# Performance work log

Measured on AMD Instinct MI355X. Metric: run time of the kernel, lower is better.

Reference implementation:

```python
import jax, jax.numpy as jnp
import numpy as np

N_NODES = 100000
N_EDGES = 1600000
IN_FEATS = 64
HIDDEN = 32
OUT_FEATS = 40


def _linear_init(key, fan_in, fan_out):
    kw, kb = jax.random.split(key)
    bound = 1.0 / np.sqrt(fan_in)
    W = jax.random.uniform(kw, (fan_in, fan_out), jnp.float32, -bound, bound)
    b = jax.random.uniform(kb, (fan_out,), jnp.float32, -bound, bound)
    return W, b


def setup_inputs() -> dict:
    key = jax.random.key(0)
    ks = jax.random.split(key, 8)
    x = jax.random.normal(ks[0], (N_NODES, IN_FEATS), jnp.float32)
    edge_index = jax.random.randint(ks[1], (2, N_EDGES), 0, N_NODES, jnp.int64)
    W_self1, b_self1 = _linear_init(ks[2], IN_FEATS, HIDDEN)
    W_neigh1, b_neigh1 = _linear_init(ks[3], IN_FEATS, HIDDEN)
    W_self2, b_self2 = _linear_init(ks[4], HIDDEN, HIDDEN)
    W_neigh2, b_neigh2 = _linear_init(ks[5], HIDDEN, HIDDEN)
    W_out, b_out = _linear_init(ks[6], HIDDEN, OUT_FEATS)
    W_lin1, b_lin1 = _linear_init(ks[7], IN_FEATS, OUT_FEATS)
    return {"x": x, "edge_index": edge_index,
            "W_self1": W_self1, "b_self1": b_self1,
            "W_neigh1": W_neigh1, "b_neigh1": b_neigh1,
            "W_self2": W_self2, "b_self2": b_self2,
            "W_neigh2": W_neigh2, "b_neigh2": b_neigh2,
            "W_out": W_out, "b_out": b_out,
            "W_lin1": W_lin1, "b_lin1": b_lin1}


def _scatter_mean(feats, src, dst, num_nodes):
    # gather neighbor features [E, F], sum into destinations, divide by degree
    msgs = feats[src]
    agg = jax.ops.segment_sum(msgs, dst, num_segments=num_nodes)
    cnt = jax.ops.segment_sum(jnp.ones((src.shape[0],), feats.dtype), dst,
                              num_segments=num_nodes)
    return agg / jnp.maximum(cnt, 1.0)[:, None]


def _intra_conv(h, src, dst, W_self, b_self, W_neigh, b_neigh, num_nodes):
    # scatter-mean aggregation + fused linear/residual(self)/relu
    x_self = h @ W_self + b_self
    neigh = _scatter_mean(h, src, dst, num_nodes)
    out = neigh @ W_neigh + b_neigh + x_self
    return jax.nn.relu(out)


def reference(x, edge_index, W_self1, b_self1, W_neigh1, b_neigh1,
              W_self2, b_self2, W_neigh2, b_neigh2, W_out, b_out,
              W_lin1, b_lin1):
    num_nodes = x.shape[0]
    src, dst = edge_index[0], edge_index[1]  # PyG source_to_target flow
    initial_x = x @ W_lin1 + b_lin1  # computed in original forward (unused in output)
    h = _intra_conv(x, src, dst, W_self1, b_self1, W_neigh1, b_neigh1, num_nodes)
    h = _intra_conv(h, src, dst, W_self2, b_self2, W_neigh2, b_neigh2, num_nodes)
    # hidden dim == 32 so x32 is the last layer's output (== h); dropout is eval no-op
    x32 = h
    logits = h @ W_out + b_out
    return (x32, logits)
```

## Files before the change

### kernel.cpp

```cpp
#include <hip/hip_runtime.h>

#define NN 100000
#define NE 1600000
#define RB 256
#define NPB 391
#define CAP 8192

typedef unsigned int uint;
typedef unsigned short ushort;
typedef __fp16 fp16x2 __attribute__((ext_vector_type(2)));

__device__ __forceinline__ float blo(uint u){ return __uint_as_float(u << 16); }
__device__ __forceinline__ float bhi(uint u){ return __uint_as_float(u & 0xffff0000u); }
__device__ __forceinline__ float b2f(ushort u){ return __uint_as_float(((uint)u) << 16); }
__device__ __forceinline__ ushort f2b(float f){
  uint u = __float_as_uint(f);
  uint r = (u + 0x7fffu + ((u >> 16) & 1u)) >> 16;
  return (ushort)r;
}
__device__ __forceinline__ uint packh2(float a, float b){
  union { fp16x2 h; uint u; } c; c.h = __builtin_amdgcn_cvt_pkrtz(a, b); return c.u;
}
__device__ __forceinline__ float h2lo(uint u){
  union { uint u; fp16x2 h; } c; c.u = u; return (float)c.h.x;
}
__device__ __forceinline__ float h2hi(uint u){
  union { uint u; fp16x2 h; } c; c.u = u; return (float)c.h.y;
}
__device__ __forceinline__ float ldf(const void* p, int i, bool isb){
  return isb ? b2f(((const ushort*)p)[i]) : ((const float*)p)[i];
}

__global__ void prep_k(const uint* __restrict__ xw,  const int* __restrict__ ei,
                       const void* __restrict__ Ws1, const void* __restrict__ bs1,
                       const void* __restrict__ Wn1, const void* __restrict__ bn1,
                       const void* __restrict__ Ws2, const void* __restrict__ bs2,
                       const void* __restrict__ Wn2, const void* __restrict__ bn2,
                       const void* __restrict__ Wo,  const void* __restrict__ bo,
                       float* __restrict__ wc1, float* __restrict__ bc1,
                       float* __restrict__ wc2, float* __restrict__ bc2,
                       float* __restrict__ wof, float* __restrict__ bof,
                       float* __restrict__ bn1f, float* __restrict__ bn2f,
                       int* __restrict__ flags, int* __restrict__ gcur)
{
  int t = threadIdx.x;
  __shared__ int nz, bcnt;
  __shared__ int s_isb, s_ei64;
  if (t == 0) { nz = 0; bcnt = 0; }
  __syncthreads();

  int hiw = ei[2 * t + 1];
  if (hiw != 0) atomicOr(&nz, 1);

  uint u = xw[t];
  uint le = (u >> 7) & 0xFFu;
  if (le == 0u || (le >= 96u && le <= 144u)) atomicAdd(&bcnt, 1);
  __syncthreads();
  if (t == 0) {
    s_ei64 = (nz == 0) ? 1 : 0;
    s_isb  = (bcnt >= 240) ? 1 : 0;
    flags[0] = s_isb;
    flags[1] = s_ei64;
  }
  __syncthreads();
  bool isb = (s_isb != 0);

  gcur[t] = t * CAP;

  for (int i = t; i < 64 * 64; i += 256) {
    int f = i >> 6, j = i & 63;
    wc1[i] = (j < 32) ? ldf(Ws1, f * 32 + j, isb) : ldf(Wn1, f * 32 + (j - 32), isb);
  }
  for (int i = t; i < 64; i += 256) bc1[i] = (i < 32) ? ldf(bs1, i, isb) : 0.f;
  for (int i = t; i < 32 * 64; i += 256) {
    int f = i >> 6, j = i & 63;
    wc2[i] = (j < 32) ? ldf(Ws2, f * 32 + j, isb) : ldf(Wn2, f * 32 + (j - 32), isb);
  }
  for (int i = t; i < 64; i += 256) bc2[i] = (i < 32) ? ldf(bs2, i, isb) : 0.f;
  for (int i = t; i < 32 * 40; i += 256) wof[i] = ldf(Wo, i, isb);
  for (int i = t; i < 40; i += 256) bof[i] = ldf(bo, i, isb);
  for (int i = t; i < 32; i += 256) bn1f[i] = ldf(bn1, i, isb);
  for (int i = t; i < 32; i += 256) bn2f[i] = ldf(bn2, i, isb);
}

__global__ __launch_bounds__(256) void part_k(const int* __restrict__ ei,
                                              const int* __restrict__ flags,
                                              int2* __restrict__ pairs,
                                              int* __restrict__ gcur, int E)
{
  __shared__ int hist[RB];
  __shared__ int gbase[RB];
  int m = flags[1];
  int base = blockIdx.x * 2048;
  hist[threadIdx.x] = 0;
  __syncthreads();
  int bk[8], rk[8]; int2 prs[8];
#pragma unroll
  for (int k = 0; k < 8; k++) {
    int e = base + threadIdx.x + k * 256;
    bk[k] = -1;
    if (e < E) {
      int d = m ? ei[2 * (E + e)] : ei[E + e];
      int s = m ? ei[2 * e] : ei[e];
      bk[k] = d / NPB;
      rk[k] = atomicAdd(&hist[bk[k]], 1);
      prs[k] = make_int2(d, s);
    }
  }
  __syncthreads();
  if (hist[threadIdx.x] > 0)
    gbase[threadIdx.x] = atomicAdd(&gcur[threadIdx.x], hist[threadIdx.x]);
  __syncthreads();
#pragma unroll
  for (int k = 0; k < 8; k++) {
    if (bk[k] >= 0) {
      int pos = gbase[bk[k]] + rk[k];
      if (pos < (bk[k] + 1) * CAP) pairs[pos] = prs[k];
    }
  }
}

__global__ void boffscan_k(const int* __restrict__ gcur, int* __restrict__ cnt,
                           int* __restrict__ boff, int* __restrict__ rowptr, int E)
{
  __shared__ int ps[RB];
  int t = threadIdx.x;
  int c = min(gcur[t] - t * CAP, CAP);
  cnt[t] = c;
  ps[t] = c;
  __syncthreads();
  for (int off = 1; off < RB; off <<= 1) {
    int v = (t >= off) ? ps[t - off] : 0;
    __syncthreads();
    ps[t] += v;
    __syncthreads();
  }
  boff[t] = ps[t] - c;
  if (t == RB - 1) rowptr[NN] = E;
}

__global__ __launch_bounds__(512) void csr_bucket_k(const int2* __restrict__ pairs,
                                                    const int* __restrict__ cnt,
                                                    const int* __restrict__ boff,
                                                    int* __restrict__ rowptr,
                                                    int* __restrict__ col)
{
  __shared__ int lh[NPB];
  __shared__ int ps[512];
  int t = threadIdx.x;
  int r = blockIdx.x;
  int lo = r * NPB;
  int nn = min(NPB, NN - lo);
  int b0 = r * CAP;
  int n = cnt[r];
  int base = boff[r];
  for (int j = t; j < NPB; j += 512) lh[j] = 0;
  __syncthreads();
  for (int i = b0 + t; i < b0 + n; i += 512)
    atomicAdd(&lh[pairs[i].x - lo], 1);
  __syncthreads();
  int v = (t < nn) ? lh[t] : 0;
  ps[t] = v;
  __syncthreads();
  for (int off = 1; off < 512; off <<= 1) {
    int x = (t >= off) ? ps[t - off] : 0;
    __syncthreads();
    ps[t] += x;
    __syncthreads();
  }
  int excl = base + ps[t] - v;
  if (t < nn) rowptr[lo + t] = excl;
  __syncthreads();
  if (t < nn) lh[t] = excl;
  __syncthreads();
  for (int i = b0 + t; i < b0 + n; i += 512) {
    int2 pr = pairs[i];
    int p = atomicAdd(&lh[pr.x - lo], 1);
    col[p] = pr.y;
  }
}

template <int IN, bool XDYN>
__global__ __launch_bounds__(256) void transform_split_k(const void* __restrict__ xin,
                                                         const float* __restrict__ W,
                                                         const float* __restrict__ bias,
                                                         float* __restrict__ tself,
                                                         uint* __restrict__ tneigh,
                                                         const int* __restrict__ flags, int N)
{
  int n = blockIdx.x * 256 + threadIdx.x;
  if (n >= N) return;
  bool isb = XDYN ? (flags[0] != 0) : false;
  float xr[IN];
  if (XDYN && isb) {
    const uint4* p = (const uint4*)((const ushort*)xin + (size_t)n * IN);
#pragma unroll
    for (int k = 0; k < IN / 8; k++) {
      uint4 v = p[k];
      xr[8 * k + 0] = blo(v.x); xr[8 * k + 1] = bhi(v.x);
      xr[8 * k + 2] = blo(v.y); xr[8 * k + 3] = bhi(v.y);
      xr[8 * k + 4] = blo(v.z); xr[8 * k + 5] = bhi(v.z);
      xr[8 * k + 6] = blo(v.w); xr[8 * k + 7] = bhi(v.w);
    }
  } else {
    const float4* p = (const float4*)((const float*)xin + (size_t)n * IN);
#pragma unroll
    for (int k = 0; k < IN / 4; k++) {
      float4 v = p[k];
      xr[4 * k + 0] = v.x; xr[4 * k + 1] = v.y; xr[4 * k + 2] = v.z; xr[4 * k + 3] = v.w;
    }
  }
#pragma unroll 1
  for (int j0 = 0; j0 < 64; j0 += 32) {
    float acc[32];
#pragma unroll
    for (int jj = 0; jj < 32; jj++) acc[jj] = bias[j0 + jj];
#pragma unroll 8
    for (int f = 0; f < IN; f++) {
      float xv = xr[f];
#pragma unroll
      for (int jj = 0; jj < 32; jj++)
        acc[jj] = fmaf(xv, W[f * 64 + j0 + jj], acc[jj]);
    }
    if (j0 == 0) {
      float* o = tself + (size_t)n * 32;
#pragma unroll
      for (int q = 0; q < 8; q++)
        ((float4*)o)[q] = make_float4(acc[4 * q], acc[4 * q + 1], acc[4 * q + 2], acc[4 * q + 3]);
    } else {
      uint* o = tneigh + (size_t)n * 16;
#pragma unroll
      for (int q = 0; q < 4; q++) {
        uint4 v;
        v.x = packh2(acc[8 * q + 0], acc[8 * q + 1]);
        v.y = packh2(acc[8 * q + 2], acc[8 * q + 3]);
        v.z = packh2(acc[8 * q + 4], acc[8 * q + 5]);
        v.w = packh2(acc[8 * q + 6], acc[8 * q + 7]);
        ((uint4*)o)[q] = v;
      }
    }
  }
}

template <int IN, int OUT, int CHUNK>
__global__ __launch_bounds__(256) void transform_k(const float* __restrict__ xin,
                                                   const float* __restrict__ W,
                                                   const float* __restrict__ bias,
                                                   void* __restrict__ xout,
                                                   const int* __restrict__ flags,
                                                   long long eoff, int N)
{
  int n = blockIdx.x * 256 + threadIdx.x;
  if (n >= N) return;
  bool isb = (flags[0] != 0);
  float xr[IN];
  const float4* p = (const float4*)(xin + (size_t)n * IN);
#pragma unroll
  for (int k = 0; k < IN / 4; k++) {
    float4 v = p[k];
    xr[4 * k + 0] = v.x; xr[4 * k + 1] = v.y; xr[4 * k + 2] = v.z; xr[4 * k + 3] = v.w;
  }
#pragma unroll 1
  for (int j0 = 0; j0 < OUT; j0 += CHUNK) {
    float acc[CHUNK];
#pragma unroll
    for (int jj = 0; jj < CHUNK; jj++) acc[jj] = bias[j0 + jj];
#pragma unroll 8
    for (int f = 0; f < IN; f++) {
      float xv = xr[f];
#pragma unroll
      for (int jj = 0; jj < CHUNK; jj++)
        acc[jj] = fmaf(xv, W[f * OUT + j0 + jj], acc[jj]);
    }
    if (isb) {
      uint* o = (uint*)((ushort*)xout + eoff + (size_t)n * OUT + j0);
#pragma unroll
      for (int q = 0; q < CHUNK / 2; q++)
        o[q] = (uint)f2b(acc[2 * q]) | ((uint)f2b(acc[2 * q + 1]) << 16);
    } else {
      float* o = (float*)xout + eoff + (size_t)n * OUT + j0;
#pragma unroll
      for (int q = 0; q < CHUNK / 4; q++)
        ((float4*)o)[q] = make_float4(acc[4 * q], acc[4 * q + 1], acc[4 * q + 2], acc[4 * q + 3]);
    }
  }
}

__global__ __launch_bounds__(256) void aggregate_k(const float* __restrict__ tself,
                                                   const uint* __restrict__ tneigh,
                                                   const int* __restrict__ rowptr,
                                                   const int* __restrict__ col,
                                                   const float* __restrict__ bneigh,
                                                   float* __restrict__ hout,
                                                   void* __restrict__ out2,
                                                   const int* __restrict__ flags, int N)
{
  int d = blockIdx.x * 4 + (threadIdx.x >> 6);
  if (d >= N) return;
  int lane = threadIdx.x & 63;
  int slot = lane >> 4, f2 = lane & 15;
  int start = rowptr[d], end = rowptr[d + 1];
  int deg = end - start;
  float a0 = 0.f, a1 = 0.f;
  for (int base = start; base < end; base += 64) {
    int cnt = min(64, end - base);
    int ce = (lane < cnt) ? col[base + lane] : 0;
#pragma unroll 1
    for (int j = 0; j < cnt; j += 8) {
      int k0 = j + slot, k1 = j + 4 + slot;
      int i0 = __shfl(ce, k0, 64);
      int i1 = __shfl(ce, k1, 64);
      if (k0 < cnt) { uint u = tneigh[(size_t)i0 * 16 + f2]; a0 += h2lo(u); a1 += h2hi(u); }
      if (k1 < cnt) { uint u = tneigh[(size_t)i1 * 16 + f2]; a0 += h2lo(u); a1 += h2hi(u); }
    }
  }
  a0 += __shfl_down(a0, 32, 64); a1 += __shfl_down(a1, 32, 64);
  a0 += __shfl_down(a0, 16, 64); a1 += __shfl_down(a1, 16, 64);
  if (lane < 16) {
    float scale = 1.0f / (float)max(deg, 1);
    float2 self = ((const float2*)(tself + (size_t)d * 32))[f2];
    float v0 = fmaxf(fmaf(a0, scale, bneigh[2 * f2]     + self.x), 0.f);
    float v1 = fmaxf(fmaf(a1, scale, bneigh[2 * f2 + 1] + self.y), 0.f);
    ((float2*)(hout + (size_t)d * 32))[f2] = make_float2(v0, v1);
    if (out2) {
      if (flags[0] != 0)
        ((uint*)out2)[(size_t)d * 16 + f2] = (uint)f2b(v0) | ((uint)f2b(v1) << 16);
      else
        ((float2*)out2)[(size_t)d * 16 + f2] = make_float2(v0, v1);
    }
  }
}

extern "C" void kernel_launch(void* const* d_in, const int* in_sizes, int n_in,
                              void* d_out, int out_size, void* d_ws, size_t ws_size,
                              hipStream_t stream)
{
  const int N = NN, E = NE;
  const void* x   = d_in[0];
  const int*  ei  = (const int*)d_in[1];

  char* p = (char*)d_ws;
  auto alloc = [&](size_t bytes) -> void* {
    void* r = (void*)p;
    p += (bytes + 255) & ~(size_t)255;
    return r;
  };
  float* wc1  = (float*)alloc(64 * 64 * 4);
  float* bc1  = (float*)alloc(64 * 4);
  float* wc2  = (float*)alloc(32 * 64 * 4);
  float* bc2  = (float*)alloc(64 * 4);
  float* wof  = (float*)alloc(32 * 40 * 4);
  float* bof  = (float*)alloc(40 * 4);
  float* bn1f = (float*)alloc(32 * 4);
  float* bn2f = (float*)alloc(32 * 4);
  int*   flags = (int*)alloc(8);
  int*   gcur = (int*)alloc(RB * 4);
  int*   cnt  = (int*)alloc(RB * 4);
  int*   boff = (int*)alloc(RB * 4);
  int*   rowptr = (int*)alloc(((size_t)N + 1) * 4);
  int*   col  = (int*)alloc((size_t)E * 4);
  int2*  pairs = (int2*)alloc((size_t)RB * CAP * 8);
  float* tself  = (float*)alloc((size_t)N * 32 * 4);
  uint*  tneigh = (uint*)alloc((size_t)N * 16 * 4);
  float* hbuf = (float*)alloc((size_t)N * 32 * 4);

  prep_k<<<1, 256, 0, stream>>>((const uint*)x, ei,
                                d_in[2], d_in[3], d_in[4], d_in[5],
                                d_in[6], d_in[7], d_in[8], d_in[9],
                                d_in[10], d_in[11],
                                wc1, bc1, wc2, bc2, wof, bof, bn1f, bn2f,
                                flags, gcur);
  part_k<<<(E + 2047) / 2048, 256, 0, stream>>>(ei, flags, pairs, gcur, E);
  boffscan_k<<<1, RB, 0, stream>>>(gcur, cnt, boff, rowptr, E);
  csr_bucket_k<<<RB, 512, 0, stream>>>(pairs, cnt, boff, rowptr, col);

  transform_split_k<64, true><<<(N + 255) / 256, 256, 0, stream>>>(
      x, wc1, bc1, tself, tneigh, flags, N);
  aggregate_k<<<(N + 3) / 4, 256, 0, stream>>>(tself, tneigh, rowptr, col, bn1f,
                                               hbuf, (void*)nullptr, flags, N);

  transform_split_k<32, false><<<(N + 255) / 256, 256, 0, stream>>>(
      hbuf, wc2, bc2, tself, tneigh, flags, N);
  aggregate_k<<<(N + 3) / 4, 256, 0, stream>>>(tself, tneigh, rowptr, col, bn2f,
                                               hbuf, d_out, flags, N);

  transform_k<32, 40, 40><<<(N + 255) / 256, 256, 0, stream>>>(
      hbuf, wof, bof, d_out, flags, (long long)N * 32, N);
}
```

Before: 314.8 us.

## Fuse output projection into second aggregate and bucket offset scan into CSR build

The final 32x40 output linear layer is folded into the second aggregation kernel, which stages each node's hidden vector in shared memory and computes the logits directly, so the intermediate hidden buffer is never written or read back. The separate single-block offset scan is merged into csr_bucket_k, where every block redundantly scans the 256 bucket counts; this removes two launches. The gather loop is also unrolled to four independent loads per iteration to raise memory-level parallelism. The grid now uses N/4 with no bounds check, which relies on N being divisible by 4.

```diff
diff --git a/kernel.cpp b/kernel.cpp
--- a/kernel.cpp
+++ b/kernel.cpp
@@ -120,40 +120,34 @@
   }
 }
 
-__global__ void boffscan_k(const int* __restrict__ gcur, int* __restrict__ cnt,
-                           int* __restrict__ boff, int* __restrict__ rowptr, int E)
-{
-  __shared__ int ps[RB];
-  int t = threadIdx.x;
-  int c = min(gcur[t] - t * CAP, CAP);
-  cnt[t] = c;
-  ps[t] = c;
-  __syncthreads();
-  for (int off = 1; off < RB; off <<= 1) {
-    int v = (t >= off) ? ps[t - off] : 0;
-    __syncthreads();
-    ps[t] += v;
-    __syncthreads();
-  }
-  boff[t] = ps[t] - c;
-  if (t == RB - 1) rowptr[NN] = E;
-}
-
 __global__ __launch_bounds__(512) void csr_bucket_k(const int2* __restrict__ pairs,
-                                                    const int* __restrict__ cnt,
-                                                    const int* __restrict__ boff,
+                                                    const int* __restrict__ gcur,
                                                     int* __restrict__ rowptr,
                                                     int* __restrict__ col)
 {
   __shared__ int lh[NPB];
   __shared__ int ps[512];
+  __shared__ int cs[RB];
   int t = threadIdx.x;
   int r = blockIdx.x;
+  if (t < RB) cs[t] = min(gcur[t] - t * CAP, CAP);
+  __syncthreads();
+  if (t < RB) ps[t] = cs[t];
+  __syncthreads();
+  for (int off = 1; off < RB; off <<= 1) {
+    int v = (t < RB && t >= off) ? ps[t - off] : 0;
+    __syncthreads();
+    if (t < RB) ps[t] += v;
+    __syncthreads();
+  }
+  int n    = cs[r];
+  int base = ps[r] - n;
+  if (r == 0 && t == 0) rowptr[NN] = NE;
+  __syncthreads();
+
   int lo = r * NPB;
   int nn = min(NPB, NN - lo);
   int b0 = r * CAP;
-  int n = cnt[r];
-  int base = boff[r];
   for (int j = t; j < NPB; j += 512) lh[j] = 0;
   __syncthreads();
   for (int i = b0 + t; i < b0 + n; i += 512)
@@ -242,50 +236,6 @@
   }
 }
 
-template <int IN, int OUT, int CHUNK>
-__global__ __launch_bounds__(256) void transform_k(const float* __restrict__ xin,
-                                                   const float* __restrict__ W,
-                                                   const float* __restrict__ bias,
-                                                   void* __restrict__ xout,
-                                                   const int* __restrict__ flags,
-                                                   long long eoff, int N)
-{
-  int n = blockIdx.x * 256 + threadIdx.x;
-  if (n >= N) return;
-  bool isb = (flags[0] != 0);
-  float xr[IN];
-  const float4* p = (const float4*)(xin + (size_t)n * IN);
-#pragma unroll
-  for (int k = 0; k < IN / 4; k++) {
-    float4 v = p[k];
-    xr[4 * k + 0] = v.x; xr[4 * k + 1] = v.y; xr[4 * k + 2] = v.z; xr[4 * k + 3] = v.w;
-  }
-#pragma unroll 1
-  for (int j0 = 0; j0 < OUT; j0 += CHUNK) {
-    float acc[CHUNK];
-#pragma unroll
-    for (int jj = 0; jj < CHUNK; jj++) acc[jj] = bias[j0 + jj];
-#pragma unroll 8
-    for (int f = 0; f < IN; f++) {
-      float xv = xr[f];
-#pragma unroll
-      for (int jj = 0; jj < CHUNK; jj++)
-        acc[jj] = fmaf(xv, W[f * OUT + j0 + jj], acc[jj]);
-    }
-    if (isb) {
-      uint* o = (uint*)((ushort*)xout + eoff + (size_t)n * OUT + j0);
-#pragma unroll
-      for (int q = 0; q < CHUNK / 2; q++)
-        o[q] = (uint)f2b(acc[2 * q]) | ((uint)f2b(acc[2 * q + 1]) << 16);
-    } else {
-      float* o = (float*)xout + eoff + (size_t)n * OUT + j0;
-#pragma unroll
-      for (int q = 0; q < CHUNK / 4; q++)
-        ((float4*)o)[q] = make_float4(acc[4 * q], acc[4 * q + 1], acc[4 * q + 2], acc[4 * q + 3]);
-    }
-  }
-}
-
 __global__ __launch_bounds__(256) void aggregate_k(const float* __restrict__ tself,
                                                    const uint* __restrict__ tneigh,
                                                    const int* __restrict__ rowptr,
@@ -293,10 +243,13 @@
                                                    const float* __restrict__ bneigh,
                                                    float* __restrict__ hout,
                                                    void* __restrict__ out2,
+                                                   const float* __restrict__ Wo,
+                                                   const float* __restrict__ bo,
                                                    const int* __restrict__ flags, int N)
 {
-  int d = blockIdx.x * 4 + (threadIdx.x >> 6);
-  if (d >= N) return;
+  __shared__ float hsh[4][32];
+  int w = threadIdx.x >> 6;
+  int d = blockIdx.x * 4 + w;
   int lane = threadIdx.x & 63;
   int slot = lane >> 4, f2 = lane & 15;
   int start = rowptr[d], end = rowptr[d + 1];
@@ -306,27 +259,46 @@
     int cnt = min(64, end - base);
     int ce = (lane < cnt) ? col[base + lane] : 0;
 #pragma unroll 1
-    for (int j = 0; j < cnt; j += 8) {
-      int k0 = j + slot, k1 = j + 4 + slot;
+    for (int j = 0; j < cnt; j += 16) {
+      int k0 = j + slot, k1 = j + 4 + slot, k2 = j + 8 + slot, k3 = j + 12 + slot;
       int i0 = __shfl(ce, k0, 64);
       int i1 = __shfl(ce, k1, 64);
-      if (k0 < cnt) { uint u = tneigh[(size_t)i0 * 16 + f2]; a0 += h2lo(u); a1 += h2hi(u); }
-      if (k1 < cnt) { uint u = tneigh[(size_t)i1 * 16 + f2]; a0 += h2lo(u); a1 += h2hi(u); }
+      int i2 = __shfl(ce, k2, 64);
+      int i3 = __shfl(ce, k3, 64);
+      uint u0 = 0, u1 = 0, u2 = 0, u3 = 0;
+      if (k0 < cnt) u0 = tneigh[(size_t)i0 * 16 + f2];
+      if (k1 < cnt) u1 = tneigh[(size_t)i1 * 16 + f2];
+      if (k2 < cnt) u2 = tneigh[(size_t)i2 * 16 + f2];
+      if (k3 < cnt) u3 = tneigh[(size_t)i3 * 16 + f2];
+      a0 += h2lo(u0) + h2lo(u1) + h2lo(u2) + h2lo(u3);
+      a1 += h2hi(u0) + h2hi(u1) + h2hi(u2) + h2hi(u3);
     }
   }
   a0 += __shfl_down(a0, 32, 64); a1 += __shfl_down(a1, 32, 64);
   a0 += __shfl_down(a0, 16, 64); a1 += __shfl_down(a1, 16, 64);
+  bool isb = (flags[0] != 0);
   if (lane < 16) {
     float scale = 1.0f / (float)max(deg, 1);
     float2 self = ((const float2*)(tself + (size_t)d * 32))[f2];
     float v0 = fmaxf(fmaf(a0, scale, bneigh[2 * f2]     + self.x), 0.f);
     float v1 = fmaxf(fmaf(a1, scale, bneigh[2 * f2 + 1] + self.y), 0.f);
-    ((float2*)(hout + (size_t)d * 32))[f2] = make_float2(v0, v1);
+    if (hout) ((float2*)(hout + (size_t)d * 32))[f2] = make_float2(v0, v1);
     if (out2) {
-      if (flags[0] != 0)
-        ((uint*)out2)[(size_t)d * 16 + f2] = (uint)f2b(v0) | ((uint)f2b(v1) << 16);
-      else
-        ((float2*)out2)[(size_t)d * 16 + f2] = make_float2(v0, v1);
+      if (isb) ((uint*)out2)[(size_t)d * 16 + f2] = (uint)f2b(v0) | ((uint)f2b(v1) << 16);
+      else     ((float2*)out2)[(size_t)d * 16 + f2] = make_float2(v0, v1);
+    }
+    hsh[w][2 * f2] = v0; hsh[w][2 * f2 + 1] = v1;
+  }
+  if (Wo) {
+    __syncthreads();
+    if (lane < 40) {
+      float acc = bo[lane];
+#pragma unroll 8
+      for (int f = 0; f < 32; f++)
+        acc = fmaf(hsh[w][f], Wo[f * 40 + lane], acc);
+      size_t idx = (size_t)N * 32 + (size_t)d * 40 + lane;
+      if (isb) ((ushort*)out2)[idx] = f2b(acc);
+      else     ((float*)out2)[idx] = acc;
     }
   }
 }
@@ -355,8 +327,6 @@
   float* bn2f = (float*)alloc(32 * 4);
   int*   flags = (int*)alloc(8);
   int*   gcur = (int*)alloc(RB * 4);
-  int*   cnt  = (int*)alloc(RB * 4);
-  int*   boff = (int*)alloc(RB * 4);
   int*   rowptr = (int*)alloc(((size_t)N + 1) * 4);
   int*   col  = (int*)alloc((size_t)E * 4);
   int2*  pairs = (int2*)alloc((size_t)RB * CAP * 8);
@@ -371,19 +341,18 @@
                                 wc1, bc1, wc2, bc2, wof, bof, bn1f, bn2f,
                                 flags, gcur);
   part_k<<<(E + 2047) / 2048, 256, 0, stream>>>(ei, flags, pairs, gcur, E);
-  boffscan_k<<<1, RB, 0, stream>>>(gcur, cnt, boff, rowptr, E);
-  csr_bucket_k<<<RB, 512, 0, stream>>>(pairs, cnt, boff, rowptr, col);
+  csr_bucket_k<<<RB, 512, 0, stream>>>(pairs, gcur, rowptr, col);
 
   transform_split_k<64, true><<<(N + 255) / 256, 256, 0, stream>>>(
       x, wc1, bc1, tself, tneigh, flags, N);
-  aggregate_k<<<(N + 3) / 4, 256, 0, stream>>>(tself, tneigh, rowptr, col, bn1f,
-                                               hbuf, (void*)nullptr, flags, N);
+  aggregate_k<<<N / 4, 256, 0, stream>>>(tself, tneigh, rowptr, col, bn1f,
+                                         hbuf, (void*)nullptr,
+                                         (const float*)nullptr, (const float*)nullptr,
+                                         flags, N);
 
   transform_split_k<32, false><<<(N + 255) / 256, 256, 0, stream>>>(
       hbuf, wc2, bc2, tself, tneigh, flags, N);
-  aggregate_k<<<(N + 3) / 4, 256, 0, stream>>>(tself, tneigh, rowptr, col, bn2f,
-                                               hbuf, d_out, flags, N);
-
-  transform_k<32, 40, 40><<<(N + 255) / 256, 256, 0, stream>>>(
-      hbuf, wof, bof, d_out, flags, (long long)N * 32, N);
-}
+  aggregate_k<<<N / 4, 256, 0, stream>>>(tself, tneigh, rowptr, col, bn2f,
+                                         (float*)nullptr, d_out,
+                                         wof, bof, flags, N);
+}
```

Result: faster. 296.3 us (-5.9%).
